# Kernel tuning notes

Measured on AMD Instinct MI355X. Metric: run time of the kernel, lower is better.

The kernel has to match this reference:

```python
import jax, jax.numpy as jnp
import numpy as np

B, S, D, H = 1, 4096, 768, 12
HD = D // H  # 64

def setup_inputs() -> dict:
    key = jax.random.key(0)
    k1, k2, k3 = jax.random.split(key, 3)
    x = jax.random.normal(k1, (B, S, D), dtype=jnp.float32)
    W_attn = jax.random.normal(k2, (D, 3 * D), dtype=jnp.float32) * 0.02
    b_attn = jnp.zeros((3 * D,), dtype=jnp.float32)
    W_proj = jax.random.normal(k3, (D, D), dtype=jnp.float32) * 0.02
    b_proj = jnp.zeros((D,), dtype=jnp.float32)
    return {"x": x, "W_attn": W_attn, "b_attn": b_attn, "W_proj": W_proj, "b_proj": b_proj}

def reference(x, W_attn, b_attn, W_proj, b_proj):
    # qkv projection (Conv1D = x @ W + b)
    qkv = x @ W_attn + b_attn  # [B,S,3D]
    q, k, v = jnp.split(qkv, 3, axis=-1)
    def split_heads(t):
        return t.reshape(B, S, H, HD).transpose(0, 2, 1, 3)  # [B,H,S,HD]
    q, k, v = split_heads(q), split_heads(k), split_heads(v)
    # NOTE: original applies no 1/sqrt(head_dim) scaling
    scores = jnp.einsum('bhqd,bhkd->bhqk', q, k)  # [B,H,S,S]
    causal = jnp.tril(jnp.ones((S, S), dtype=bool))
    mask_value = jnp.finfo(scores.dtype).min
    scores = jnp.where(causal, scores, mask_value)
    attn = jax.nn.softmax(scores, axis=-1)
    # dropout is identity in eval mode
    out = jnp.einsum('bhqk,bhkd->bhqd', attn, v)  # [B,H,S,HD]
    out = out.transpose(0, 2, 1, 3).reshape(B, S, D)
    return out @ W_proj + b_proj
```

## Files before the change

kernel.cpp:

```cpp
#include <hip/hip_runtime.h>


typedef short bf16x8 __attribute__((ext_vector_type(8)));
typedef float f32x4 __attribute__((ext_vector_type(4)));
typedef unsigned short u16x8_t __attribute__((ext_vector_type(8)));
typedef unsigned short u16x4_t __attribute__((ext_vector_type(4)));

#define ATT_S  4096
#define ATT_D  768
#define ATT_3D 2304
#define ATT_H  12
#define LOG2E  1.44269504089f
#define NUM_UNITS 1920

__device__ __forceinline__ unsigned short f2b(float f) {
  union { float f; unsigned int u; } v; v.f = f;
  unsigned int r = v.u + 0x7fffu + ((v.u >> 16) & 1u);
  return (unsigned short)(r >> 16);
}
__device__ __forceinline__ float b2f(unsigned short b) {
  union { unsigned int u; float f; } v; v.u = ((unsigned int)b) << 16;
  return v.f;
}
__device__ __forceinline__ unsigned int cvtpk(float a, float b) {
  unsigned int r;
  asm("v_cvt_pk_bf16_f32 %0, %1, %2" : "=v"(r) : "v"(a), "v"(b));
  return r;
}

__device__ __forceinline__ f32x4 mfma16(bf16x8 a, bf16x8 b, f32x4 c) {
  return __builtin_amdgcn_mfma_f32_16x16x32_bf16(a, b, c, 0, 0, 0);
}

__device__ __forceinline__ void glds16(const void* g, void* l) {
  __builtin_amdgcn_global_load_lds((__attribute__((address_space(1))) void*)g,
                                   (__attribute__((address_space(3))) void*)l,
                                   16, 0, 0);
}

__device__ __forceinline__ void lbar() {
  asm volatile("s_waitcnt lgkmcnt(0)" ::: "memory");
  __builtin_amdgcn_s_barrier();
}

__device__ __forceinline__ int swz8(int row, int c) {
  return row * 64 + ((c ^ (row & 7)) << 3);
}


__global__ __launch_bounds__(256) void convert_f32_bf16(
    const float* __restrict__ in, unsigned short* __restrict__ out, int n4) {
  int i = blockIdx.x * 256 + threadIdx.x;
  if (i >= n4) return;
  float4 v = ((const float4*)in)[i];
  u16x4_t o;
  o[0] = f2b(v.x); o[1] = f2b(v.y); o[2] = f2b(v.z); o[3] = f2b(v.w);
  ((u16x4_t*)out)[i] = o;
}

__global__ __launch_bounds__(256) void transpose_conv(
    const float* __restrict__ W, unsigned short* __restrict__ WT, int K, int N) {
  __shared__ float tile[32][33];
  int bx = blockIdx.x, by = blockIdx.y;
  int tx = threadIdx.x & 31, ty = threadIdx.x >> 5;
#pragma unroll
  for (int k = 0; k < 4; k++)
    tile[ty + k * 8][tx] = W[(size_t)(by * 32 + ty + k * 8) * N + bx * 32 + tx];
  __syncthreads();
#pragma unroll
  for (int k = 0; k < 4; k++)
    WT[(size_t)(bx * 32 + ty + k * 8) * K + by * 32 + tx] = f2b(tile[tx][ty + k * 8]);
}


template <int BF16_OUT>
__global__ __launch_bounds__(256) void gemm_bias(
    const unsigned short* __restrict__ A, const unsigned short* __restrict__ Bt,
    const float* __restrict__ bias, void* __restrict__ Cout,
    int M, int N, int K) {
  __shared__ unsigned short As[128 * 32];
  __shared__ unsigned short Bs[128 * 32];
  const int t = threadIdx.x;
  const int lane = t & 63;
  const int wave = t >> 6;
  const int wr = wave >> 1, wc = wave & 1;
  const int rl = lane & 15, rg = lane >> 4;

  const int nbn = N >> 7;
  const int nwg = gridDim.x;
  const int bid = blockIdx.x;
  const int cpx = nwg >> 3;
  const int swz = (bid & 7) * cpx + (bid >> 3);
  const int bm = swz / nbn, bn = swz % nbn;

  const unsigned short* Ab = A + (size_t)bm * 128 * K;
  const unsigned short* Bb = Bt + (size_t)bn * 128 * K;

  f32x4 acc[4][4];
#pragma unroll
  for (int m = 0; m < 4; m++)
#pragma unroll
    for (int n = 0; n < 4; n++) acc[m][n] = (f32x4){0.f, 0.f, 0.f, 0.f};

  for (int kt = 0; kt < K; kt += 32) {
    if (kt) __syncthreads();
#pragma unroll
    for (int it = 0; it < 2; ++it) {
      int idx = it * 256 + t;
      int row = idx >> 2;
      int slot = idx & 3;
      int sl2 = slot ^ ((row >> 1) & 3);
      unsigned short* ldsA = As + (size_t)(it * 256 + wave * 64) * 8;
      unsigned short* ldsB = Bs + (size_t)(it * 256 + wave * 64) * 8;
      glds16(Ab + (size_t)row * K + kt + sl2 * 8, ldsA);
      glds16(Bb + (size_t)row * K + kt + sl2 * 8, ldsB);
    }
    __syncthreads();

    bf16x8 a[4], b[4];
#pragma unroll
    for (int m = 0; m < 4; m++) {
      int row = wr * 64 + m * 16 + rl;
      int sl2 = rg ^ ((row >> 1) & 3);
      a[m] = *(const bf16x8*)&As[row * 32 + sl2 * 8];
    }
#pragma unroll
    for (int n = 0; n < 4; n++) {
      int row = wc * 64 + n * 16 + rl;
      int sl2 = rg ^ ((row >> 1) & 3);
      b[n] = *(const bf16x8*)&Bs[row * 32 + sl2 * 8];
    }
#pragma unroll
    for (int m = 0; m < 4; m++)
#pragma unroll
      for (int n = 0; n < 4; n++)
        acc[m][n] = mfma16(a[m], b[n], acc[m][n]);
  }

#pragma unroll
  for (int n = 0; n < 4; n++) {
    int col = bn * 128 + wc * 64 + n * 16 + rl;
    float bv = bias[col];
#pragma unroll
    for (int m = 0; m < 4; m++) {
      int row0 = bm * 128 + wr * 64 + m * 16 + rg * 4;
#pragma unroll
      for (int i = 0; i < 4; i++) {
        float v = acc[m][n][i] + bv;
        if (BF16_OUT)
          ((unsigned short*)Cout)[(size_t)(row0 + i) * N + col] = f2b(v);
        else
          ((float*)Cout)[(size_t)(row0 + i) * N + col] = v;
      }
    }
  }
}


__global__ __launch_bounds__(256) void attn_fwd(
    const unsigned short* __restrict__ qkv, unsigned short* __restrict__ aout,
    unsigned short* __restrict__ pscr, float* __restrict__ ml,
    unsigned int* __restrict__ qctr) {
  __shared__ unsigned short Kb[64 * 64];
  __shared__ unsigned short Vb[64 * 64];
  __shared__ unsigned short Ps[4][16 * 64];
  __shared__ int sticket;

  const int tid = threadIdx.x;
  const int lane = tid & 63;
  const int w = tid >> 6;
  const int rl = lane & 15, rg = lane >> 4;

  unsigned short* Pw = Ps[w];
  const int skey = lane >> 3;
  const int slot = lane & 7;

  for (;;) {
    if (tid == 0) sticket = (int)atomicAdd(qctr, 1u);
    __syncthreads();
    const int tk = sticket;
    if (tk >= NUM_UNITS) return;

    const int h = tk % ATT_H;
    const int u = 159 - (tk / ATT_H);
    int qb, ck;
    if (u < 16)      { qb = u;                    ck = 0; }
    else if (u < 48) { qb = 16 + ((u - 16) >> 1); ck = (u - 16) & 1; }
    else if (u < 96) { qb = 32 + (u - 48) / 3;    ck = (u - 48) % 3; }
    else             { qb = 48 + ((u - 96) >> 2); ck = (u - 96) & 3; }

    const int nt = qb + 1;
    const int t0 = ck * 16;
    const int t1 = min(nt, t0 + 16);
    const int qbase = qb * 64 + w * 16;

    bf16x8 qf[2];
#pragma unroll
    for (int ks = 0; ks < 2; ks++)
      qf[ks] = *(const bf16x8*)&qkv[(size_t)(qbase + rl) * ATT_3D + h * 64 + ks * 32 + rg * 8];

    float mS = -3.0e38f, lS = 0.f;
    f32x4 oacc[4];
#pragma unroll
    for (int hf = 0; hf < 4; hf++) oacc[hf] = (f32x4){0.f, 0.f, 0.f, 0.f};

    u16x8_t kr[2], vr[2];
    const size_t gstep = (size_t)64 * ATT_3D;
    const size_t gbase = (size_t)(w * 8 + skey) * ATT_3D + 768 + h * 64 + slot * 8;

    {
      const size_t gb = gbase + (size_t)t0 * gstep;
      kr[0] = *(const u16x8_t*)&qkv[gb];
      kr[1] = *(const u16x8_t*)&qkv[gb + 32 * ATT_3D];
      vr[0] = *(const u16x8_t*)&qkv[gb + 768];
      vr[1] = *(const u16x8_t*)&qkv[gb + 32 * ATT_3D + 768];
#pragma unroll
      for (int it = 0; it < 2; ++it) {
        int key = it * 32 + w * 8 + skey;
        *(u16x8_t*)&Kb[swz8(key, slot)] = kr[it];
        *(u16x8_t*)&Pw[swz8(it * 8 + skey, slot)] = vr[it];
      }
#pragma unroll
      for (int kk = 0; kk < 2; ++kk) {
        u16x8_t g;
#pragma unroll
        for (int j = 0; j < 8; j++)
          g[j] = Pw[swz8(kk * 8 + j, lane >> 3) + (lane & 7)];
        *(u16x8_t*)&Vb[swz8(lane, kk * 4 + w)] = g;
      }
    }
    lbar();

    for (int t = t0; t < t1; ++t) {
      const bool pref = (t + 1 < t1);
      if (pref) {
        const size_t gb = gbase + (size_t)(t + 1) * gstep;
        kr[0] = *(const u16x8_t*)&qkv[gb];
        kr[1] = *(const u16x8_t*)&qkv[gb + 32 * ATT_3D];
        vr[0] = *(const u16x8_t*)&qkv[gb + 768];
        vr[1] = *(const u16x8_t*)&qkv[gb + 32 * ATT_3D + 768];
      }

      f32x4 st[4];
#pragma unroll
      for (int kf = 0; kf < 4; kf++) st[kf] = (f32x4){0.f, 0.f, 0.f, 0.f};
      __builtin_amdgcn_s_setprio(1);
#pragma unroll
      for (int ks = 0; ks < 2; ks++) {
#pragma unroll
        for (int kf = 0; kf < 4; kf++) {
          bf16x8 kfr = *(const bf16x8*)&Kb[swz8(kf * 16 + rl, ks * 4 + rg)];
          st[kf] = mfma16(kfr, qf[ks], st[kf]);
        }
      }
      __builtin_amdgcn_s_setprio(0);

      lbar();
      if (pref) {
#pragma unroll
        for (int it = 0; it < 2; ++it)
          *(u16x8_t*)&Kb[swz8(it * 32 + w * 8 + skey, slot)] = kr[it];
      }

      if (t == nt - 1) {
#pragma unroll
        for (int kf = 0; kf < 4; kf++)
#pragma unroll
          for (int i = 0; i < 4; i++) {
            int key = t * 64 + kf * 16 + rg * 4 + i;
            if (key > qbase + rl) st[kf][i] = -3.0e38f;
          }
      }

      float pm = fmaxf(fmaxf(st[0][0], st[0][1]), fmaxf(st[0][2], st[0][3]));
#pragma unroll
      for (int kf = 1; kf < 4; kf++)
        pm = fmaxf(pm, fmaxf(fmaxf(st[kf][0], st[kf][1]),
                             fmaxf(st[kf][2], st[kf][3])));
      pm = fmaxf(pm, __shfl_xor(pm, 16, 64));
      pm = fmaxf(pm, __shfl_xor(pm, 32, 64));
      if (!__all(pm - mS <= 8.f)) {
        float mn = fmaxf(mS, pm);
        float fac = __expf(mS - mn);
        mS = mn;
        lS *= fac;
#pragma unroll
        for (int i = 0; i < 4; i++) {
          float fi = __shfl(fac, rg * 4 + i, 64);
#pragma unroll
          for (int hf = 0; hf < 4; hf++) oacc[hf][i] *= fi;
        }
      }
      const float mC = mS * LOG2E;
      float psum = 0.f;
#pragma unroll
      for (int kf = 0; kf < 4; kf++) {
        float p0 = __builtin_amdgcn_exp2f(fmaf(st[kf][0], LOG2E, -mC));
        float p1 = __builtin_amdgcn_exp2f(fmaf(st[kf][1], LOG2E, -mC));
        float p2 = __builtin_amdgcn_exp2f(fmaf(st[kf][2], LOG2E, -mC));
        float p3 = __builtin_amdgcn_exp2f(fmaf(st[kf][3], LOG2E, -mC));
        psum += (p0 + p1) + (p2 + p3);
        uint2 d;
        d.x = cvtpk(p0, p1);
        d.y = cvtpk(p2, p3);
        *(u16x4_t*)&Pw[swz8(rl, kf * 2 + (rg >> 1)) + (rg & 1) * 4] =
            __builtin_bit_cast(u16x4_t, d);
      }
      psum += __shfl_xor(psum, 16, 64);
      psum += __shfl_xor(psum, 32, 64);
      lS += psum;

      __builtin_amdgcn_s_setprio(1);
#pragma unroll
      for (int ks2 = 0; ks2 < 2; ks2++) {
        bf16x8 pa = *(const bf16x8*)&Pw[swz8(rl, ks2 * 4 + rg)];
#pragma unroll
        for (int hf = 0; hf < 4; hf++) {
          bf16x8 vbf = *(const bf16x8*)&Vb[swz8(hf * 16 + rl, ks2 * 4 + rg)];
          oacc[hf] = mfma16(pa, vbf, oacc[hf]);
        }
      }
      __builtin_amdgcn_s_setprio(0);

      lbar();
      if (pref) {
#pragma unroll
        for (int it = 0; it < 2; ++it)
          *(u16x8_t*)&Pw[swz8(it * 8 + skey, slot)] = vr[it];
#pragma unroll
        for (int kk = 0; kk < 2; ++kk) {
          u16x8_t g;
#pragma unroll
          for (int j = 0; j < 8; j++)
            g[j] = Pw[swz8(kk * 8 + j, lane >> 3) + (lane & 7)];
          *(u16x8_t*)&Vb[swz8(lane, kk * 4 + w)] = g;
        }
      }
    }

    const bool split = (qb >= 16);
    unsigned short* dst;
    int pitch;
    if (!split || ck == 0) {
      dst = aout + (size_t)(qb * 64) * ATT_D + h * 64;
      pitch = ATT_D;
    } else {
      int s;
      if (qb < 32)      s = h * 96 + (qb - 16);
      else if (qb < 48) s = h * 96 + 16 + (qb - 32) * 2 + (ck - 1);
      else              s = h * 96 + 48 + (qb - 48) * 3 + (ck - 1);
      dst = pscr + (size_t)s * 4096;
      pitch = 64;
    }
    if (split && rg == 0) {
      int unit = h * 48 + (qb - 16);
      float2* mlp = (float2*)ml;
      mlp[(unit * 4 + ck) * 64 + w * 16 + rl] = make_float2(mS, lS);
    }
#pragma unroll
    for (int i = 0; i < 4; i++) {
      float li = __shfl(lS, rg * 4 + i, 64);
      float inv = 1.f / li;
      int qrow = w * 16 + rg * 4 + i;
#pragma unroll
      for (int hf = 0; hf < 4; hf++)
        dst[(size_t)qrow * pitch + hf * 16 + rl] = f2b(oacc[hf][i] * inv);
    }
    __syncthreads();
  }
}


__global__ __launch_bounds__(256) void attn_combine(
    const unsigned short* __restrict__ pscr, const float* __restrict__ ml,
    unsigned short* __restrict__ ao) {
  const int unit = blockIdx.x;
  const int h = unit / 48, uqb = unit % 48, qb = uqb + 16;
  const int nch = (qb + 16) >> 4;
  const int tid = threadIdx.x;
  const int q = tid >> 2, part = tid & 3;

  const float2* mlp = (const float2*)ml;
  float m[4], l[4];
  float M = -3.0e38f;
  for (int c = 0; c < nch; ++c) {
    float2 p = mlp[(unit * 4 + c) * 64 + q];
    m[c] = p.x; l[c] = p.y;
    M = fmaxf(M, m[c]);
  }
  float wgt[4], den = 0.f;
  for (int c = 0; c < nch; ++c) {
    wgt[c] = l[c] * __expf(m[c] - M);
    den += wgt[c];
  }

  float acc[16];
#pragma unroll
  for (int j = 0; j < 16; j++) acc[j] = 0.f;

  unsigned short* aorow = ao + (size_t)(qb * 64 + q) * ATT_D + h * 64 + part * 16;
  for (int c = 0; c < nch; ++c) {
    const unsigned short* src;
    if (c == 0) {
      src = aorow;
    } else {
      int s;
      if (qb < 32)      s = h * 96 + (qb - 16);
      else if (qb < 48) s = h * 96 + 16 + (qb - 32) * 2 + (c - 1);
      else              s = h * 96 + 48 + (qb - 48) * 3 + (c - 1);
      src = pscr + (size_t)s * 4096 + q * 64 + part * 16;
    }
    u16x8_t v0 = *(const u16x8_t*)src;
    u16x8_t v1 = *(const u16x8_t*)(src + 8);
#pragma unroll
    for (int j = 0; j < 8; j++) acc[j] += wgt[c] * b2f(v0[j]);
#pragma unroll
    for (int j = 0; j < 8; j++) acc[8 + j] += wgt[c] * b2f(v1[j]);
  }
  float inv = 1.f / den;
  u16x8_t o0, o1;
#pragma unroll
  for (int j = 0; j < 8; j++) { o0[j] = f2b(acc[j] * inv); o1[j] = f2b(acc[8 + j] * inv); }
  *(u16x8_t*)aorow = o0;
  *(u16x8_t*)(aorow + 8) = o1;
}


extern "C" void kernel_launch(void* const* d_in, const int* in_sizes, int n_in,
                              void* d_out, int out_size, void* d_ws, size_t ws_size,
                              hipStream_t stream) {
  const float* x      = (const float*)d_in[0];
  const float* W_attn = (const float*)d_in[1];
  const float* b_attn = (const float*)d_in[2];
  const float* W_proj = (const float*)d_in[3];
  const float* b_proj = (const float*)d_in[4];
  float* out = (float*)d_out;

  char* ws = (char*)d_ws;
  unsigned short* xb  = (unsigned short*)(ws);
  unsigned short* WaT = (unsigned short*)(ws + 6291456);
  unsigned short* WpT = (unsigned short*)(ws + 9830400);
  unsigned short* qkv = (unsigned short*)(ws + 11010048);
  unsigned short* ao  = (unsigned short*)(ws + 29884416);
  unsigned short* pscr = (unsigned short*)(ws);
  unsigned int*   qctr = (unsigned int*)(ws + 9437184);
  float*          ml   = (float*)(ws + 9830400);

  convert_f32_bf16<<<3072, 256, 0, stream>>>(x, xb, 786432);
  transpose_conv<<<dim3(72, 24), 256, 0, stream>>>(W_attn, WaT, 768, 2304);

  gemm_bias<1><<<576, 256, 0, stream>>>(xb, WaT, b_attn, qkv, 4096, 2304, 768);
  hipMemsetAsync(qctr, 0, 4, stream);
  attn_fwd<<<1536, 256, 0, stream>>>(qkv, ao, pscr, ml, qctr);
  attn_combine<<<576, 256, 0, stream>>>(pscr, ml, ao);

  transpose_conv<<<dim3(24, 24), 256, 0, stream>>>(W_proj, WpT, 768, 768);
  gemm_bias<0><<<192, 256, 0, stream>>>(ao, WpT, b_proj, out, 4096, 768, 768);
}
```

Baseline: 149.1 us.

## Switch attention to 32x32 MFMA with 128-row query blocks and static grid

```diff
diff --git a/kernel.cpp b/kernel.cpp
--- a/kernel.cpp
+++ b/kernel.cpp
@@ -2,16 +2,17 @@
 
 
 typedef short bf16x8 __attribute__((ext_vector_type(8)));
-typedef float f32x4 __attribute__((ext_vector_type(4)));
+typedef float f32x16 __attribute__((ext_vector_type(16)));
 typedef unsigned short u16x8_t __attribute__((ext_vector_type(8)));
 typedef unsigned short u16x4_t __attribute__((ext_vector_type(4)));
+typedef unsigned int   u32x4_t __attribute__((ext_vector_type(4)));
+typedef float f32x4 __attribute__((ext_vector_type(4)));
 
 #define ATT_S  4096
 #define ATT_D  768
 #define ATT_3D 2304
 #define ATT_H  12
 #define LOG2E  1.44269504089f
-#define NUM_UNITS 1920
 
 __device__ __forceinline__ unsigned short f2b(float f) {
   union { float f; unsigned int u; } v; v.f = f;
@@ -30,6 +31,9 @@
 
 __device__ __forceinline__ f32x4 mfma16(bf16x8 a, bf16x8 b, f32x4 c) {
   return __builtin_amdgcn_mfma_f32_16x16x32_bf16(a, b, c, 0, 0, 0);
+}
+__device__ __forceinline__ f32x16 mfma32(bf16x8 a, bf16x8 b, f32x16 c) {
+  return __builtin_amdgcn_mfma_f32_32x32x16_bf16(a, b, c, 0, 0, 0);
 }
 
 __device__ __forceinline__ void glds16(const void* g, void* l) {
@@ -159,125 +163,116 @@
 
 __global__ __launch_bounds__(256) void attn_fwd(
     const unsigned short* __restrict__ qkv, unsigned short* __restrict__ aout,
-    unsigned short* __restrict__ pscr, float* __restrict__ ml,
-    unsigned int* __restrict__ qctr) {
+    unsigned short* __restrict__ pscr, float* __restrict__ ml) {
   __shared__ unsigned short Kb[64 * 64];
-  __shared__ unsigned short Vb[64 * 64];
-  __shared__ unsigned short Ps[4][16 * 64];
-  __shared__ int sticket;
+  __shared__ unsigned short Vt[64 * 64];
+  __shared__ unsigned short Vrow[64 * 64];
 
   const int tid = threadIdx.x;
   const int lane = tid & 63;
   const int w = tid >> 6;
-  const int rl = lane & 15, rg = lane >> 4;
-
-  unsigned short* Pw = Ps[w];
-  const int skey = lane >> 3;
-  const int slot = lane & 7;
-
-  for (;;) {
-    if (tid == 0) sticket = (int)atomicAdd(qctr, 1u);
-    __syncthreads();
-    const int tk = sticket;
-    if (tk >= NUM_UNITS) return;
-
-    const int h = tk % ATT_H;
-    const int u = 159 - (tk / ATT_H);
-    int qb, ck;
-    if (u < 16)      { qb = u;                    ck = 0; }
-    else if (u < 48) { qb = 16 + ((u - 16) >> 1); ck = (u - 16) & 1; }
-    else if (u < 96) { qb = 32 + (u - 48) / 3;    ck = (u - 48) % 3; }
-    else             { qb = 48 + ((u - 96) >> 2); ck = (u - 96) & 3; }
-
-    const int nt = qb + 1;
-    const int t0 = ck * 16;
-    const int t1 = min(nt, t0 + 16);
-    const int qbase = qb * 64 + w * 16;
-
-    bf16x8 qf[2];
-#pragma unroll
-    for (int ks = 0; ks < 2; ks++)
-      qf[ks] = *(const bf16x8*)&qkv[(size_t)(qbase + rl) * ATT_3D + h * 64 + ks * 32 + rg * 8];
-
-    float mS = -3.0e38f, lS = 0.f;
-    f32x4 oacc[4];
-#pragma unroll
-    for (int hf = 0; hf < 4; hf++) oacc[hf] = (f32x4){0.f, 0.f, 0.f, 0.f};
-
-    u16x8_t kr[2], vr[2];
-    const size_t gstep = (size_t)64 * ATT_3D;
-    const size_t gbase = (size_t)(w * 8 + skey) * ATT_3D + 768 + h * 64 + slot * 8;
-
-    {
-      const size_t gb = gbase + (size_t)t0 * gstep;
+  const int l31 = lane & 31, h5 = lane >> 5;
+
+  const int bid = blockIdx.x;
+  const int h = bid % ATT_H;
+  const int u = 79 - (bid / ATT_H);
+  int sb, ck;
+  if (u < 8)       { sb = u;                    ck = 0; }
+  else if (u < 24) { sb = 8 + ((u - 8) >> 1);   ck = (u - 8) & 1; }
+  else if (u < 48) { sb = 16 + (u - 24) / 3;    ck = (u - 24) % 3; }
+  else             { sb = 24 + ((u - 48) >> 2); ck = (u - 48) & 3; }
+
+  const int nt = 2 * sb + 2;
+  const int t0 = ck * 16;
+  const int t1 = min(nt, t0 + 16);
+  const int q = sb * 128 + w * 32 + l31;
+
+  const int skey = tid >> 3;
+  const int slot = tid & 7;
+
+  bf16x8 qf[4];
+#pragma unroll
+  for (int ks = 0; ks < 4; ks++)
+    qf[ks] = *(const bf16x8*)&qkv[(size_t)q * ATT_3D + h * 64 + ks * 16 + h5 * 8];
+
+  float mS = -3.0e38f, lS = 0.f;
+  f32x16 oa0 = (f32x16)(0.f), oa1 = (f32x16)(0.f);
+
+  u16x8_t kr[2], vr[2];
+  const size_t gstep = (size_t)64 * ATT_3D;
+  const size_t gbase = (size_t)skey * ATT_3D + 768 + h * 64 + slot * 8;
+
+  {
+    const size_t gb = gbase + (size_t)t0 * gstep;
+    kr[0] = *(const u16x8_t*)&qkv[gb];
+    kr[1] = *(const u16x8_t*)&qkv[gb + 32 * ATT_3D];
+    vr[0] = *(const u16x8_t*)&qkv[gb + 768];
+    vr[1] = *(const u16x8_t*)&qkv[gb + 32 * ATT_3D + 768];
+#pragma unroll
+    for (int p = 0; p < 2; ++p) {
+      *(u16x8_t*)&Kb[swz8(p * 32 + skey, slot)] = kr[p];
+      *(u16x8_t*)&Vrow[swz8(p * 32 + skey, slot)] = vr[p];
+    }
+#pragma unroll
+    for (int kk = 0; kk < 2; ++kk) {
+      int kb = w + kk * 4;
+      u16x8_t g;
+#pragma unroll
+      for (int j = 0; j < 8; j++)
+        g[j] = Vrow[swz8(kb * 8 + j, lane >> 3) + (lane & 7)];
+      *(u16x8_t*)&Vt[swz8(lane, kb)] = g;
+    }
+  }
+  lbar();
+
+  for (int t = t0; t < t1; ++t) {
+    const bool pref = (t + 1 < t1);
+    const bool active = (t * 64 <= sb * 128 + w * 32 + 31);
+    if (pref) {
+      const size_t gb = gbase + (size_t)(t + 1) * gstep;
       kr[0] = *(const u16x8_t*)&qkv[gb];
       kr[1] = *(const u16x8_t*)&qkv[gb + 32 * ATT_3D];
       vr[0] = *(const u16x8_t*)&qkv[gb + 768];
       vr[1] = *(const u16x8_t*)&qkv[gb + 32 * ATT_3D + 768];
-#pragma unroll
-      for (int it = 0; it < 2; ++it) {
-        int key = it * 32 + w * 8 + skey;
-        *(u16x8_t*)&Kb[swz8(key, slot)] = kr[it];
-        *(u16x8_t*)&Pw[swz8(it * 8 + skey, slot)] = vr[it];
-      }
-#pragma unroll
-      for (int kk = 0; kk < 2; ++kk) {
-        u16x8_t g;
-#pragma unroll
-        for (int j = 0; j < 8; j++)
-          g[j] = Pw[swz8(kk * 8 + j, lane >> 3) + (lane & 7)];
-        *(u16x8_t*)&Vb[swz8(lane, kk * 4 + w)] = g;
-      }
-    }
+    }
+
+    f32x16 st[2];
+    st[0] = (f32x16)(0.f); st[1] = (f32x16)(0.f);
+    if (active) {
+      __builtin_amdgcn_s_setprio(1);
+#pragma unroll
+      for (int kg = 0; kg < 2; kg++)
+#pragma unroll
+        for (int ks = 0; ks < 4; ks++) {
+          bf16x8 kfr = *(const bf16x8*)&Kb[swz8(kg * 32 + l31, ks * 2 + h5)];
+          st[kg] = mfma32(kfr, qf[ks], st[kg]);
+        }
+      __builtin_amdgcn_s_setprio(0);
+    }
+
     lbar();
-
-    for (int t = t0; t < t1; ++t) {
-      const bool pref = (t + 1 < t1);
-      if (pref) {
-        const size_t gb = gbase + (size_t)(t + 1) * gstep;
-        kr[0] = *(const u16x8_t*)&qkv[gb];
-        kr[1] = *(const u16x8_t*)&qkv[gb + 32 * ATT_3D];
-        vr[0] = *(const u16x8_t*)&qkv[gb + 768];
-        vr[1] = *(const u16x8_t*)&qkv[gb + 32 * ATT_3D + 768];
-      }
-
-      f32x4 st[4];
-#pragma unroll
-      for (int kf = 0; kf < 4; kf++) st[kf] = (f32x4){0.f, 0.f, 0.f, 0.f};
-      __builtin_amdgcn_s_setprio(1);
-#pragma unroll
-      for (int ks = 0; ks < 2; ks++) {
-#pragma unroll
-        for (int kf = 0; kf < 4; kf++) {
-          bf16x8 kfr = *(const bf16x8*)&Kb[swz8(kf * 16 + rl, ks * 4 + rg)];
-          st[kf] = mfma16(kfr, qf[ks], st[kf]);
-        }
-      }
-      __builtin_amdgcn_s_setprio(0);
-
-      lbar();
-      if (pref) {
-#pragma unroll
-        for (int it = 0; it < 2; ++it)
-          *(u16x8_t*)&Kb[swz8(it * 32 + w * 8 + skey, slot)] = kr[it];
-      }
-
-      if (t == nt - 1) {
-#pragma unroll
-        for (int kf = 0; kf < 4; kf++)
-#pragma unroll
-          for (int i = 0; i < 4; i++) {
-            int key = t * 64 + kf * 16 + rg * 4 + i;
-            if (key > qbase + rl) st[kf][i] = -3.0e38f;
+    if (pref) {
+#pragma unroll
+      for (int p = 0; p < 2; ++p)
+        *(u16x8_t*)&Kb[swz8(p * 32 + skey, slot)] = kr[p];
+    }
+
+    if (active) {
+      if (t * 64 + 63 > sb * 128 + w * 32) {
+#pragma unroll
+        for (int kg = 0; kg < 2; kg++)
+#pragma unroll
+          for (int r = 0; r < 16; r++) {
+            int key = t * 64 + kg * 32 + (r & 3) + 8 * (r >> 2) + 4 * h5;
+            if (key > q) st[kg][r] = -3.0e38f;
           }
       }
 
-      float pm = fmaxf(fmaxf(st[0][0], st[0][1]), fmaxf(st[0][2], st[0][3]));
-#pragma unroll
-      for (int kf = 1; kf < 4; kf++)
-        pm = fmaxf(pm, fmaxf(fmaxf(st[kf][0], st[kf][1]),
-                             fmaxf(st[kf][2], st[kf][3])));
-      pm = fmaxf(pm, __shfl_xor(pm, 16, 64));
+      float pm = st[0][0];
+#pragma unroll
+      for (int r = 1; r < 16; r++) pm = fmaxf(pm, st[0][r]);
+#pragma unroll
+      for (int r = 0; r < 16; r++) pm = fmaxf(pm, st[1][r]);
       pm = fmaxf(pm, __shfl_xor(pm, 32, 64));
       if (!__all(pm - mS <= 8.f)) {
         float mn = fmaxf(mS, pm);
@@ -285,89 +280,97 @@
         mS = mn;
         lS *= fac;
 #pragma unroll
-        for (int i = 0; i < 4; i++) {
-          float fi = __shfl(fac, rg * 4 + i, 64);
-#pragma unroll
-          for (int hf = 0; hf < 4; hf++) oacc[hf][i] *= fi;
-        }
+        for (int r = 0; r < 16; r++) { oa0[r] *= fac; oa1[r] *= fac; }
       }
       const float mC = mS * LOG2E;
       float psum = 0.f;
 #pragma unroll
-      for (int kf = 0; kf < 4; kf++) {
-        float p0 = __builtin_amdgcn_exp2f(fmaf(st[kf][0], LOG2E, -mC));
-        float p1 = __builtin_amdgcn_exp2f(fmaf(st[kf][1], LOG2E, -mC));
-        float p2 = __builtin_amdgcn_exp2f(fmaf(st[kf][2], LOG2E, -mC));
-        float p3 = __builtin_amdgcn_exp2f(fmaf(st[kf][3], LOG2E, -mC));
-        psum += (p0 + p1) + (p2 + p3);
-        uint2 d;
-        d.x = cvtpk(p0, p1);
-        d.y = cvtpk(p2, p3);
-        *(u16x4_t*)&Pw[swz8(rl, kf * 2 + (rg >> 1)) + (rg & 1) * 4] =
-            __builtin_bit_cast(u16x4_t, d);
-      }
-      psum += __shfl_xor(psum, 16, 64);
+      for (int kg = 0; kg < 2; kg++)
+#pragma unroll
+        for (int r = 0; r < 16; r++) {
+          float p = __builtin_amdgcn_exp2f(fmaf(st[kg][r], LOG2E, -mC));
+          st[kg][r] = p;
+          psum += p;
+        }
       psum += __shfl_xor(psum, 32, 64);
       lS += psum;
 
       __builtin_amdgcn_s_setprio(1);
 #pragma unroll
-      for (int ks2 = 0; ks2 < 2; ks2++) {
-        bf16x8 pa = *(const bf16x8*)&Pw[swz8(rl, ks2 * 4 + rg)];
-#pragma unroll
-        for (int hf = 0; hf < 4; hf++) {
-          bf16x8 vbf = *(const bf16x8*)&Vb[swz8(hf * 16 + rl, ks2 * 4 + rg)];
-          oacc[hf] = mfma16(pa, vbf, oacc[hf]);
-        }
+      for (int kc = 0; kc < 4; kc++) {
+        const int kg = kc >> 1;
+        const int rb = (kc & 1) << 3;
+        unsigned e00 = cvtpk(st[kg][rb + 0], st[kg][rb + 1]);
+        unsigned e01 = cvtpk(st[kg][rb + 2], st[kg][rb + 3]);
+        unsigned e10 = cvtpk(st[kg][rb + 4], st[kg][rb + 5]);
+        unsigned e11 = cvtpk(st[kg][rb + 6], st[kg][rb + 7]);
+        unsigned own0 = h5 ? e10 : e00, own1 = h5 ? e11 : e01;
+        unsigned snd0 = h5 ? e00 : e10, snd1 = h5 ? e01 : e11;
+        unsigned r0 = (unsigned)__shfl_xor((int)snd0, 32, 64);
+        unsigned r1 = (unsigned)__shfl_xor((int)snd1, 32, 64);
+        u32x4_t fd;
+        fd[0] = h5 ? r0 : own0; fd[1] = h5 ? r1 : own1;
+        fd[2] = h5 ? own0 : r0; fd[3] = h5 ? own1 : r1;
+        bf16x8 pfr = __builtin_bit_cast(bf16x8, fd);
+        bf16x8 v0 = *(const bf16x8*)&Vt[swz8(l31, kc * 2 + h5)];
+        bf16x8 v1 = *(const bf16x8*)&Vt[swz8(32 + l31, kc * 2 + h5)];
+        oa0 = mfma32(v0, pfr, oa0);
+        oa1 = mfma32(v1, pfr, oa1);
       }
       __builtin_amdgcn_s_setprio(0);
-
-      lbar();
-      if (pref) {
-#pragma unroll
-        for (int it = 0; it < 2; ++it)
-          *(u16x8_t*)&Pw[swz8(it * 8 + skey, slot)] = vr[it];
-#pragma unroll
-        for (int kk = 0; kk < 2; ++kk) {
-          u16x8_t g;
-#pragma unroll
-          for (int j = 0; j < 8; j++)
-            g[j] = Pw[swz8(kk * 8 + j, lane >> 3) + (lane & 7)];
-          *(u16x8_t*)&Vb[swz8(lane, kk * 4 + w)] = g;
-        }
-      }
-    }
-
-    const bool split = (qb >= 16);
-    unsigned short* dst;
-    int pitch;
-    if (!split || ck == 0) {
-      dst = aout + (size_t)(qb * 64) * ATT_D + h * 64;
-      pitch = ATT_D;
-    } else {
-      int s;
-      if (qb < 32)      s = h * 96 + (qb - 16);
-      else if (qb < 48) s = h * 96 + 16 + (qb - 32) * 2 + (ck - 1);
-      else              s = h * 96 + 48 + (qb - 48) * 3 + (ck - 1);
-      dst = pscr + (size_t)s * 4096;
-      pitch = 64;
-    }
-    if (split && rg == 0) {
-      int unit = h * 48 + (qb - 16);
-      float2* mlp = (float2*)ml;
-      mlp[(unit * 4 + ck) * 64 + w * 16 + rl] = make_float2(mS, lS);
-    }
-#pragma unroll
-    for (int i = 0; i < 4; i++) {
-      float li = __shfl(lS, rg * 4 + i, 64);
-      float inv = 1.f / li;
-      int qrow = w * 16 + rg * 4 + i;
-#pragma unroll
-      for (int hf = 0; hf < 4; hf++)
-        dst[(size_t)qrow * pitch + hf * 16 + rl] = f2b(oacc[hf][i] * inv);
-    }
-    __syncthreads();
-  }
+    }
+
+    lbar();
+    if (pref) {
+#pragma unroll
+      for (int p = 0; p < 2; ++p)
+        *(u16x8_t*)&Vrow[swz8(p * 32 + skey, slot)] = vr[p];
+#pragma unroll
+      for (int kk = 0; kk < 2; ++kk) {
+        int kb = w + kk * 4;
+        u16x8_t g;
+#pragma unroll
+        for (int j = 0; j < 8; j++)
+          g[j] = Vrow[swz8(kb * 8 + j, lane >> 3) + (lane & 7)];
+        *(u16x8_t*)&Vt[swz8(lane, kb)] = g;
+      }
+    }
+  }
+
+  const bool split = (sb >= 8);
+  unsigned short* dst;
+  int pitch;
+  if (!split || ck == 0) {
+    dst = aout + (size_t)q * ATT_D + h * 64;
+    pitch = 0;
+  } else {
+    int sbase = (sb < 16) ? (sb - 8)
+              : (sb < 24) ? 8 + (sb - 16) * 2
+                          : 24 + (sb - 24) * 3;
+    int s = h * 48 + sbase + (ck - 1);
+    dst = pscr + (size_t)s * 8192 + (w * 32 + l31) * 64;
+    pitch = 0;
+  }
+  if (split && lane < 32) {
+    int b2 = (sb < 16) ? (sb - 8) * 2
+           : (sb < 24) ? 16 + (sb - 16) * 3
+                       : 40 + (sb - 24) * 4;
+    float2* mlp = (float2*)ml;
+    mlp[(size_t)(h * 72 + b2 + ck) * 128 + w * 32 + lane] = make_float2(mS, lS);
+  }
+  const float inv = 1.f / lS;
+#pragma unroll
+  for (int hg = 0; hg < 2; hg++)
+#pragma unroll
+    for (int rq = 0; rq < 4; rq++) {
+      u16x4_t o4;
+#pragma unroll
+      for (int c = 0; c < 4; c++) {
+        float v = (hg ? oa1[rq * 4 + c] : oa0[rq * 4 + c]) * inv;
+        o4[c] = f2b(v);
+      }
+      *(u16x4_t*)&dst[hg * 32 + rq * 8 + h5 * 4] = o4;
+    }
 }
 
 
@@ -375,16 +378,23 @@
     const unsigned short* __restrict__ pscr, const float* __restrict__ ml,
     unsigned short* __restrict__ ao) {
   const int unit = blockIdx.x;
-  const int h = unit / 48, uqb = unit % 48, qb = uqb + 16;
-  const int nch = (qb + 16) >> 4;
+  const int h = unit / 24, sb = unit % 24 + 8;
+  const int nch = (sb < 16) ? 2 : (sb < 24) ? 3 : 4;
   const int tid = threadIdx.x;
-  const int q = tid >> 2, part = tid & 3;
+  const int qr = tid >> 1, part = tid & 1;
+
+  const int b2 = (sb < 16) ? (sb - 8) * 2
+               : (sb < 24) ? 16 + (sb - 16) * 3
+                           : 40 + (sb - 24) * 4;
+  const int sbase = (sb < 16) ? (sb - 8)
+                  : (sb < 24) ? 8 + (sb - 16) * 2
+                              : 24 + (sb - 24) * 3;
 
   const float2* mlp = (const float2*)ml;
   float m[4], l[4];
   float M = -3.0e38f;
   for (int c = 0; c < nch; ++c) {
-    float2 p = mlp[(unit * 4 + c) * 64 + q];
+    float2 p = mlp[(size_t)(h * 72 + b2 + c) * 128 + qr];
     m[c] = p.x; l[c] = p.y;
     M = fmaxf(M, m[c]);
   }
@@ -394,35 +404,32 @@
     den += wgt[c];
   }
 
-  float acc[16];
-#pragma unroll
-  for (int j = 0; j < 16; j++) acc[j] = 0.f;
-
-  unsigned short* aorow = ao + (size_t)(qb * 64 + q) * ATT_D + h * 64 + part * 16;
+  float acc[32];
+#pragma unroll
+  for (int j = 0; j < 32; j++) acc[j] = 0.f;
+
+  unsigned short* aorow =
+      ao + (size_t)(sb * 128 + qr) * ATT_D + h * 64 + part * 32;
   for (int c = 0; c < nch; ++c) {
-    const unsigned short* src;
-    if (c == 0) {
-      src = aorow;
-    } else {
-      int s;
-      if (qb < 32)      s = h * 96 + (qb - 16);
-      else if (qb < 48) s = h * 96 + 16 + (qb - 32) * 2 + (c - 1);
-      else              s = h * 96 + 48 + (qb - 48) * 3 + (c - 1);
-      src = pscr + (size_t)s * 4096 + q * 64 + part * 16;
-    }
-    u16x8_t v0 = *(const u16x8_t*)src;
-    u16x8_t v1 = *(const u16x8_t*)(src + 8);
-#pragma unroll
-    for (int j = 0; j < 8; j++) acc[j] += wgt[c] * b2f(v0[j]);
-#pragma unroll
-    for (int j = 0; j < 8; j++) acc[8 + j] += wgt[c] * b2f(v1[j]);
-  }
-  float inv = 1.f / den;
-  u16x8_t o0, o1;
-#pragma unroll
-  for (int j = 0; j < 8; j++) { o0[j] = f2b(acc[j] * inv); o1[j] = f2b(acc[8 + j] * inv); }
-  *(u16x8_t*)aorow = o0;
-  *(u16x8_t*)(aorow + 8) = o1;
+    const unsigned short* src =
+        (c == 0) ? aorow
+                 : pscr + (size_t)(h * 48 + sbase + (c - 1)) * 8192 +
+                       qr * 64 + part * 32;
+#pragma unroll
+    for (int v = 0; v < 4; v++) {
+      u16x8_t x = *(const u16x8_t*)(src + v * 8);
+#pragma unroll
+      for (int j = 0; j < 8; j++) acc[v * 8 + j] += wgt[c] * b2f(x[j]);
+    }
+  }
+  float invd = 1.f / den;
+#pragma unroll
+  for (int v = 0; v < 4; v++) {
+    u16x8_t o;
+#pragma unroll
+    for (int j = 0; j < 8; j++) o[j] = f2b(acc[v * 8 + j] * invd);
+    *(u16x8_t*)(aorow + v * 8) = o;
+  }
 }
 
 
@@ -443,16 +450,14 @@
   unsigned short* qkv = (unsigned short*)(ws + 11010048);
   unsigned short* ao  = (unsigned short*)(ws + 29884416);
   unsigned short* pscr = (unsigned short*)(ws);
-  unsigned int*   qctr = (unsigned int*)(ws + 9437184);
   float*          ml   = (float*)(ws + 9830400);
 
   convert_f32_bf16<<<3072, 256, 0, stream>>>(x, xb, 786432);
   transpose_conv<<<dim3(72, 24), 256, 0, stream>>>(W_attn, WaT, 768, 2304);
 
   gemm_bias<1><<<576, 256, 0, stream>>>(xb, WaT, b_attn, qkv, 4096, 2304, 768);
-  hipMemsetAsync(qctr, 0, 4, stream);
-  attn_fwd<<<1536, 256, 0, stream>>>(qkv, ao, pscr, ml, qctr);
-  attn_combine<<<576, 256, 0, stream>>>(pscr, ml, ao);
+  attn_fwd<<<960, 256, 0, stream>>>(qkv, ao, pscr, ml);
+  attn_combine<<<288, 256, 0, stream>>>(pscr, ml, ao);
 
   transpose_conv<<<dim3(24, 24), 256, 0, stream>>>(W_proj, WpT, 768, 768);
   gemm_bias<0><<<192, 256, 0, stream>>>(ao, WpT, b_proj, out, 4096, 768, 768);
```

After: 128.2 us. 14.0% less time.
